# Performance work log

Measured on AMD Instinct MI355X. Metric: run time of the kernel, lower is better.

The kernel has to match this reference:

```python
import jax, jax.numpy as jnp
import numpy as np
from jax import lax

C = 256          # fpn_feats_dim
NC = 20          # num_classes
GROUPS = 16      # GroupNorm groups
EPS = 1e-5       # GroupNorm eps (torch default)
BATCH = 8
LEVELS = [(100, 128), (50, 64), (25, 32)]  # FPN level H,W for 800x1024 image, strides 8/16/32
PRIOR_BIAS = -float(np.log((1 - 0.01) / 0.01))  # ~-4.5951, FCOS prior init


def _conv3(x, w, b):
    # 3x3 stride-1 pad-1 conv, NCHW / OIHW
    y = lax.conv_general_dilated(x, w, (1, 1), 'SAME',
                                 dimension_numbers=('NCHW', 'OIHW', 'NCHW'))
    return y + b[None, :, None, None]


def _gn(x, g, b):
    n, c, h, w = x.shape
    xr = x.reshape(n, GROUPS, c // GROUPS, h, w)
    m = xr.mean(axis=(2, 3, 4), keepdims=True)
    v = xr.var(axis=(2, 3, 4), keepdims=True)
    xr = (xr - m) * lax.rsqrt(v + EPS)
    x = xr.reshape(n, c, h, w)
    return x * g[None, :, None, None] + b[None, :, None, None]


def _forward(feat0, feat1, feat2,
             cls_conv_w, cls_conv_b, cls_gn_g, cls_gn_b, cls_out_w, cls_out_b,
             reg_conv_w, reg_conv_b, reg_gn_g, reg_gn_b,
             reg_out_w, reg_out_b, ctr_w, ctr_b):
    feats = [feat0, feat1, feat2]
    all_cls, all_reg, all_ctr = [], [], []
    for f in feats:
        n = f.shape[0]
        x = f
        for i in range(2):
            x = jax.nn.relu(_gn(_conv3(x, cls_conv_w[i], cls_conv_b[i]),
                                cls_gn_g[i], cls_gn_b[i]))
        logits = _conv3(x, cls_out_w, cls_out_b)           # [N, NC, H, W]
        # view(N,-1,NC,H,W).permute(0,3,4,1,2).reshape(N,-1,NC) == NHWC flatten
        all_cls.append(logits.transpose(0, 2, 3, 1).reshape(n, -1, NC))
        t = f
        for i in range(2):
            t = jax.nn.relu(_gn(_conv3(t, reg_conv_w[i], reg_conv_b[i]),
                                reg_gn_g[i], reg_gn_b[i]))
        # bbox_reg = Sequential(conv, ReLU), then an extra relu in forward (idempotent)
        bbox = jax.nn.relu(jax.nn.relu(_conv3(t, reg_out_w, reg_out_b)))  # [N,4,H,W]
        all_reg.append(bbox.transpose(0, 2, 3, 1).reshape(n, -1, 1))      # [N,H*W*4,1]
        ctr = _conv3(t, ctr_w, ctr_b)                                     # [N,1,H,W]
        all_ctr.append(ctr.transpose(0, 2, 3, 1).reshape(n, -1, 1))       # [N,H*W,1]
    cls_cat = jnp.concatenate(all_cls, axis=1)
    reg_cat = jnp.concatenate(all_reg, axis=1)
    ctr_cat = jnp.concatenate(all_ctr, axis=1)
    return cls_cat, reg_cat, ctr_cat


def setup_inputs() -> dict:
    key = jax.random.key(0)
    ks = jax.random.split(key, 20)
    std = 0.01
    d = {}
    for i, (h, w) in enumerate(LEVELS):
        d[f"feat{i}"] = jax.random.normal(ks[i], (BATCH, C, h, w), jnp.float32)
    # classification head params
    d["cls_conv_w"] = jax.random.normal(ks[3], (2, C, C, 3, 3), jnp.float32) * std
    d["cls_conv_b"] = jnp.zeros((2, C), jnp.float32)
    d["cls_gn_g"] = jnp.ones((2, C), jnp.float32)
    d["cls_gn_b"] = jnp.zeros((2, C), jnp.float32)
    d["cls_out_w"] = jax.random.normal(ks[4], (NC, C, 3, 3), jnp.float32) * std
    d["cls_out_b"] = jnp.full((NC,), PRIOR_BIAS, jnp.float32)
    d["reg_conv_w"] = jax.random.normal(ks[5], (2, C, C, 3, 3), jnp.float32) * std
    d["reg_conv_b"] = jnp.zeros((2, C), jnp.float32)
    d["reg_gn_g"] = jnp.ones((2, C), jnp.float32)
    d["reg_gn_b"] = jnp.zeros((2, C), jnp.float32)
    d["reg_out_w"] = jax.random.normal(ks[6], (4, C, 3, 3), jnp.float32) * std
    d["reg_out_b"] = jnp.zeros((4,), jnp.float32)
    d["ctr_w"] = jax.random.normal(ks[7], (1, C, 3, 3), jnp.float32) * std
    d["ctr_b"] = jnp.zeros((1,), jnp.float32)
    return d


def reference(feat0, feat1, feat2,
              cls_conv_w, cls_conv_b, cls_gn_g, cls_gn_b, cls_out_w, cls_out_b,
              reg_conv_w, reg_conv_b, reg_gn_g, reg_gn_b,
              reg_out_w, reg_out_b, ctr_w, ctr_b):
    return _forward(feat0, feat1, feat2,
                    cls_conv_w, cls_conv_b, cls_gn_g, cls_gn_b, cls_out_w, cls_out_b,
                    reg_conv_w, reg_conv_b, reg_gn_g, reg_gn_b,
                    reg_out_w, reg_out_b, ctr_w, ctr_b)
```

## Files before the change

kernel.cpp:

```cpp
#include <hip/hip_runtime.h>

typedef unsigned short u16;
typedef __attribute__((ext_vector_type(8))) unsigned short ushort8v;
typedef __attribute__((ext_vector_type(8))) short short8v;
typedef __attribute__((ext_vector_type(4))) float floatx4;

__device__ __forceinline__ float bf2f(u16 u) {
    unsigned v = ((unsigned)u) << 16;
    float f;
    __builtin_memcpy(&f, &v, 4);
    return f;
}
__device__ __forceinline__ u16 f2bf(float f) {
    unsigned v;
    __builtin_memcpy(&v, &f, 4);
    unsigned r = (v + 0x7fffu + ((v >> 16) & 1u)) >> 16;
    return (u16)r;
}
__device__ __forceinline__ float ld(const void* p, long i, int isf) {
    return isf ? ((const float*)p)[i] : bf2f(((const u16*)p)[i]);
}
__device__ __forceinline__ void gll16(const void* g, void* l) {
    __builtin_amdgcn_global_load_lds(
        (const __attribute__((address_space(1))) unsigned int*)g,
        (__attribute__((address_space(3))) unsigned int*)l, 16, 0, 0);
}

__global__ void detect_dtype(const u16* __restrict__ gng, int* __restrict__ flag) {
    if (threadIdx.x == 0) flag[0] = (gng[0] == 0x3F80u) ? 0 : 1;
}

__global__ void conv_params(const void* ccb, const void* cgg, const void* cgb,
                            const void* rcb, const void* rgg, const void* rgb,
                            const void* cob, const void* rob, const void* ctb,
                            const int* __restrict__ flag, u16* __restrict__ dst) {
    const int isf = flag[0];
    for (int i = threadIdx.x; i < 3104; i += 256) {
        const void* src; int off;
        if (i < 512)       { src = ccb; off = i; }
        else if (i < 1024) { src = cgg; off = i - 512; }
        else if (i < 1536) { src = cgb; off = i - 1024; }
        else if (i < 2048) { src = rcb; off = i - 1536; }
        else if (i < 2560) { src = rgg; off = i - 2048; }
        else if (i < 3072) { src = rgb; off = i - 2560; }
        else if (i < 3092) { src = cob; off = i - 3072; }
        else if (i < 3096) { src = rob; off = i - 3092; }
        else if (i < 3097) { src = ctb; off = 0; }
        else               { dst[i] = 0; continue; }
        dst[i] = f2bf(ld(src, off, isf));
    }
}

__global__ void prep_w(const void* __restrict__ src, long srcOff,
                       const int* __restrict__ flag, u16* __restrict__ dst,
                       int CoutSrc, int BNr) {
    const int isf = flag[0];
    unsigned e = blockIdx.x * 256 + threadIdx.x;
    unsigned c = e & 31u;
    unsigned r = (e >> 5) % (unsigned)BNr;
    unsigned kc = (e / (32u * BNr)) % 72u;
    unsigned nt = e / (32u * BNr * 72u);
    unsigned co = nt * BNr + r;
    unsigned tap = kc >> 3, ci = (kc & 7u) * 32u + c;
    u16 v = 0;
    if (co < (unsigned)CoutSrc)
        v = f2bf(ld(src, srcOff + (long)(co * 256u + ci) * 9 + tap, isf));
    dst[e] = v;
}

__global__ void prep_w_regctr(const void* __restrict__ wreg, const void* __restrict__ wctr,
                              const int* __restrict__ flag, u16* __restrict__ dst) {
    const int isf = flag[0];
    unsigned e = blockIdx.x * 256 + threadIdx.x;
    unsigned c = e & 31u;
    unsigned r = (e >> 5) & 31u;
    unsigned kc = e / 1024u;
    unsigned tap = kc >> 3, ci = (kc & 7u) * 32u + c;
    u16 v = 0;
    if (r < 4u)       v = f2bf(ld(wreg, (long)(r * 256u + ci) * 9 + tap, isf));
    else if (r == 4u) v = f2bf(ld(wctr, (long)ci * 9 + tap, isf));
    dst[e] = v;
}

__global__ void zero_border(u16* __restrict__ buf, int H, int Wp, int Hp, int NB) {
    const int nb = 2 * Wp + 2 * H;
    unsigned idx = blockIdx.x * 256 + threadIdx.x;
    unsigned ch = idx & 31u;
    unsigned rem = idx >> 5;
    unsigned n = rem / (unsigned)nb;
    unsigned b = rem - n * nb;
    if (n >= (unsigned)NB) return;
    int ppos;
    if ((int)b < Wp) ppos = (int)b;
    else if ((int)b < 2 * Wp) ppos = (Hp - 1) * Wp + ((int)b - Wp);
    else {
        int r = (int)b - 2 * Wp;
        ppos = (1 + (r >> 1)) * Wp + ((r & 1) ? (Wp - 1) : 0);
    }
    ushort8v z = {};
    *(ushort8v*)(buf + ((long)n * (Hp * Wp) + ppos) * 256 + ch * 8) = z;
}

__global__ void nchw_to_nhwc_pad(const void* __restrict__ src, long srcOff,
                                 const int* __restrict__ flag, u16* __restrict__ dst,
                                 int S, int W, int Wp, int HpWp) {
    const int isf = flag[0];
    __shared__ u16 t[64][34];
    const int tid = threadIdx.x;
    const int n = blockIdx.z, ct = blockIdx.y;
    const int s0 = blockIdx.x * 32;
    const long base = srcOff + ((long)(n * 256 + ct * 64)) * S + s0;
#pragma unroll
    for (int i = 0; i < 8; ++i) {
        int c = i * 8 + (tid >> 5);
        t[c][tid & 31] = f2bf(ld(src, base + (long)c * S + (tid & 31), isf));
    }
    __syncthreads();
#pragma unroll
    for (int i = 0; i < 8; ++i) {
        int px = i * 4 + (tid >> 6);
        int s = s0 + px;
        int y = s / W, x = s - y * W;
        dst[((long)n * HpWp + (long)(y + 1) * Wp + (x + 1)) * 256 + ct * 64 + (tid & 63)] =
            t[tid & 63][px];
    }
}

__global__ void gn_stats(const u16* __restrict__ x, float* __restrict__ stats, int S) {
    const int n = blockIdx.x >> 4, g = blockIdx.x & 15;
    const int tid = threadIdx.x;
    float sum = 0.f, sq = 0.f;
    const u16* base = x + (long)n * S * 256 + g * 16 + (tid & 7) * 2;
    for (int p = tid >> 3; p < S; p += 32) {
        unsigned v = *(const unsigned*)(base + (long)p * 256);
        float x0 = bf2f((u16)(v & 0xffffu));
        float x1 = bf2f((u16)(v >> 16));
        sum += x0 + x1;
        sq += x0 * x0 + x1 * x1;
    }
#pragma unroll
    for (int off = 32; off > 0; off >>= 1) {
        sum += __shfl_down(sum, off, 64);
        sq  += __shfl_down(sq, off, 64);
    }
    __shared__ float red[8];
    const int wave = tid >> 6, lane = tid & 63;
    if (lane == 0) { red[wave * 2] = sum; red[wave * 2 + 1] = sq; }
    __syncthreads();
    if (tid == 0) {
        stats[(n * 16 + g) * 2]     = red[0] + red[2] + red[4] + red[6];
        stats[(n * 16 + g) * 2 + 1] = red[1] + red[3] + red[5] + red[7];
    }
}

__global__ void gn_norm_relu(const u16* __restrict__ x, const float* __restrict__ stats,
                             const u16* __restrict__ gam, const u16* __restrict__ bet,
                             u16* __restrict__ outp, int S, int W, int Wp, int HpWp,
                             float invC) {
    unsigned idx = blockIdx.x * 256 + threadIdx.x;
    unsigned c8 = idx & 31u;
    unsigned rem = idx >> 5;
    unsigned p = rem % (unsigned)S;
    unsigned n = rem / (unsigned)S;
    unsigned c0 = c8 * 8u;
    unsigned g = c0 >> 4;
    float sum = stats[(n * 16 + g) * 2], sq = stats[(n * 16 + g) * 2 + 1];
    float mean = sum * invC;
    float var = fmaxf(sq * invC - mean * mean, 0.f);
    float rstd = rsqrtf(var + 1e-5f);
    ushort8v v = *(const ushort8v*)(x + ((long)(n * S + p)) * 256 + c0);
    unsigned y = p / (unsigned)W, xc = p - y * W;
    u16* dst = outp + ((long)n * HpWp + (long)(y + 1) * Wp + (xc + 1)) * 256 + c0;
    ushort8v o;
#pragma unroll
    for (int j = 0; j < 8; ++j) {
        float xv = bf2f(v[j]);
        float r = (xv - mean) * rstd * bf2f(gam[c0 + j]) + bf2f(bet[c0 + j]);
        o[j] = f2bf(fmaxf(r, 0.f));
    }
    *(ushort8v*)dst = o;
}

template <int BN, int MODE>
__global__ __launch_bounds__(256)
void conv_gemm(const u16* __restrict__ Ap, const u16* __restrict__ Wb,
               const u16* __restrict__ bias, const u16* __restrict__ bias2,
               void* __restrict__ outp, long ob1, long ob2,
               const int* __restrict__ dflag,
               int M, int n0, int S, int W, int Wp, int HpWp, int prefS) {
    static_assert(BN == 128 || BN == 32, "");
    constexpr int MI = (BN == 128) ? 4 : 2;
    constexpr int NI = (BN == 128) ? 4 : 2;
    __shared__ __align__(16) u16 ldsA[128 * 32];
    __shared__ __align__(16) u16 ldsB[BN * 32];
    const int tid = threadIdx.x;
    const int lane = tid & 63, wave = tid >> 6;
    const int m0 = blockIdx.x * 128;
    const int nt = blockIdx.y;
    int isf = 0;
    if (MODE != 0) isf = dflag[0];

    const int r0 = 32 * wave + (lane >> 2);
    int mA0 = m0 + r0;        if (mA0 > M - 1) mA0 = M - 1;
    int mA1 = m0 + r0 + 16;   if (mA1 > M - 1) mA1 = M - 1;
    const char* aL0;
    const char* aL1;
    {
        int n8 = mA0 / S, s = mA0 - n8 * S, y = s / W, x = s - y * W;
        aL0 = (const char*)(Ap + ((long)n8 * HpWp + (long)(y + 1) * Wp + (x + 1)) * 256)
              + (lane & 3) * 16;
        n8 = mA1 / S; s = mA1 - n8 * S; y = s / W; x = s - y * W;
        aL1 = (const char*)(Ap + ((long)n8 * HpWp + (long)(y + 1) * Wp + (x + 1)) * 256)
              + (lane & 3) * 16;
    }
    u16* lA0 = ldsA + (32 * wave) * 32;
    u16* lA1 = ldsA + (32 * wave + 16) * 32;

    const u16* b_tile = Wb + (long)nt * 72 * BN * 32;
    const char* bsrc;
    u16* lB0; u16* lB1;
    if (BN == 128) {
        bsrc = (const char*)b_tile + (32 * wave) * 64 + lane * 16;
        lB0 = ldsB + (32 * wave) * 32;
        lB1 = ldsB + (32 * wave + 16) * 32;
    } else {
        bsrc = (const char*)b_tile + wave * 1024 + lane * 16;
        lB0 = ldsB + wave * 16 * 32;
        lB1 = nullptr;
    }

    floatx4 acc[MI][NI] = {};

    const int wm = (BN == 128) ? (wave & 1) * 64 : wave * 32;
    const int wn = (BN == 128) ? (wave >> 1) * 64 : 0;
    const int fr = lane & 15, q = lane >> 4;
    const u16* fA = ldsA + (wm + fr) * 32 + q * 8;
    const u16* fB = ldsB + (wn + fr) * 32 + q * 8;

    for (int kc = 0; kc < 72; ++kc) {
        const int tap = kc >> 3;
        const int ty = tap / 3;
        const int tx = tap - ty * 3;
        const long aoffB = ((long)((ty - 1) * Wp + (tx - 1)) * 256 + (kc & 7) * 32) * 2;
        __syncthreads();
        gll16(aL0 + aoffB, lA0);
        gll16(aL1 + aoffB, lA1);
        if (BN == 128) {
            gll16(bsrc, lB0);
            gll16(bsrc + 1024, lB1);
            bsrc += 8192;
        } else {
            if (wave < 2) gll16(bsrc, lB0);
            bsrc += 2048;
        }
        __syncthreads();
        short8v af[MI], bf[NI];
#pragma unroll
        for (int i = 0; i < MI; ++i) af[i] = *(const short8v*)(fA + i * 16 * 32);
#pragma unroll
        for (int j = 0; j < NI; ++j) bf[j] = *(const short8v*)(fB + j * 16 * 32);
#pragma unroll
        for (int i = 0; i < MI; ++i)
#pragma unroll
            for (int j = 0; j < NI; ++j)
                acc[i][j] = __builtin_amdgcn_mfma_f32_16x16x32_bf16(af[i], bf[j],
                                                                    acc[i][j], 0, 0, 0);
    }

    if (MODE == 0) {
        u16* out = (u16*)outp;
#pragma unroll
        for (int j = 0; j < NI; ++j) {
            const int co = nt * BN + wn + j * 16 + fr;
            const float bv = bf2f(bias[co]);
#pragma unroll
            for (int i = 0; i < MI; ++i) {
#pragma unroll
                for (int r = 0; r < 4; ++r) {
                    const int mg = m0 + wm + i * 16 + q * 4 + r;
                    if (mg < M)
                        out[(long)mg * 256 + co] = f2bf(acc[i][j][r] + bv);
                }
            }
        }
    } else {
#pragma unroll
        for (int i = 0; i < MI; ++i) {
#pragma unroll
            for (int r = 0; r < 4; ++r) {
                const int mg = m0 + wm + i * 16 + q * 4 + r;
                if (mg >= M) continue;
                const int n8 = mg / S;
                const int s = mg - n8 * S;
                const long gi = n0 + n8;
#pragma unroll
                for (int j = 0; j < NI; ++j) {
                    const int co = wn + j * 16 + fr;
                    const float v = acc[i][j][r];
                    long oi = -1;
                    float val = 0.f;
                    if (MODE == 1) {
                        if (co < 20) {
                            oi = ob1 + gi * 336000 + (long)(prefS + s) * 20 + co;
                            val = v + bf2f(bias[co]);
                        }
                    } else {
                        if (co < 4) {
                            oi = ob1 + gi * 67200 + (long)(prefS + s) * 4 + co;
                            val = fmaxf(v + bf2f(bias[co]), 0.f);
                        } else if (co == 4) {
                            oi = ob2 + gi * 16800 + (prefS + s);
                            val = v + bf2f(bias2[0]);
                        }
                    }
                    if (oi >= 0) {
                        if (isf) ((float*)outp)[oi] = val;
                        else     ((u16*)outp)[oi] = f2bf(val);
                    }
                }
            }
        }
    }
}

extern "C" void kernel_launch(void* const* d_in, const int* in_sizes, int n_in,
                              void* d_out, int out_size, void* d_ws, size_t ws_size,
                              hipStream_t stream) {
    (void)in_sizes; (void)n_in; (void)out_size;
    const void* feat[3]   = {d_in[0], d_in[1], d_in[2]};
    const void* cls_conv_w = d_in[3];
    const void* cls_conv_b = d_in[4];
    const void* cls_gn_g   = d_in[5];
    const void* cls_gn_b   = d_in[6];
    const void* cls_out_w  = d_in[7];
    const void* cls_out_b  = d_in[8];
    const void* reg_conv_w = d_in[9];
    const void* reg_conv_b = d_in[10];
    const void* reg_gn_g   = d_in[11];
    const void* reg_gn_b   = d_in[12];
    const void* reg_out_w  = d_in[13];
    const void* reg_out_b  = d_in[14];
    const void* ctr_w      = d_in[15];
    const void* ctr_b      = d_in[16];

    char* ws = (char*)d_ws;
    int*  flag     = (int*)ws;
    u16*  params   = (u16*)(ws + 1024);
    u16*  Wb       = (u16*)(ws + 8192);
    float* stats   = (float*)(ws + 5021696);
    const size_t base = 5022720;
    const size_t per_img = 6789120ull + 6553600ull + 6789120ull;
    int NB = 8;
    while (NB > 1 && base + (size_t)NB * per_img > ws_size) NB >>= 1;
    u16* feat_pad  = (u16*)(ws + base);
    u16* conv_out  = (u16*)(ws + base + (size_t)NB * 6789120ull);
    u16* norm_pad  = (u16*)(ws + base + (size_t)NB * (6789120ull + 6553600ull));

    detect_dtype<<<1, 64, 0, stream>>>((const u16*)cls_gn_g, flag);
    conv_params<<<1, 256, 0, stream>>>(cls_conv_b, cls_gn_g, cls_gn_b,
                                       reg_conv_b, reg_gn_g, reg_gn_b,
                                       cls_out_b, reg_out_b, ctr_b, flag, params);
    prep_w<<<2304, 256, 0, stream>>>(cls_conv_w, 0,      flag, Wb + 0,       256, 128);
    prep_w<<<2304, 256, 0, stream>>>(cls_conv_w, 589824, flag, Wb + 589824,  256, 128);
    prep_w<<<2304, 256, 0, stream>>>(reg_conv_w, 0,      flag, Wb + 1179648, 256, 128);
    prep_w<<<2304, 256, 0, stream>>>(reg_conv_w, 589824, flag, Wb + 1769472, 256, 128);
    prep_w<<<288,  256, 0, stream>>>(cls_out_w,  0,      flag, Wb + 2359296, 20, 32);
    prep_w_regctr<<<288, 256, 0, stream>>>(reg_out_w, ctr_w, flag, Wb + 2433024);

    const int Hs[3] = {100, 50, 25}, Wss[3] = {128, 64, 32};
    const int prefSs[3] = {0, 12800, 16000};

    for (int l = 0; l < 3; ++l) {
        const int H = Hs[l], W = Wss[l], S = H * W;
        const int Hp = H + 2, Wp = W + 2, HpWp = Hp * Wp;
        const int prefS = prefSs[l];
        const int nb = 2 * Wp + 2 * H;
        const float invC = 1.0f / (16.0f * (float)S);

        for (int n0 = 0; n0 < 8; n0 += NB) {
            const int M = NB * S;
            const int mtiles = (M + 127) / 128;
            const int zb_blocks = (NB * nb * 32 + 255) / 256;

            zero_border<<<zb_blocks, 256, 0, stream>>>(feat_pad, H, Wp, Hp, NB);
            zero_border<<<zb_blocks, 256, 0, stream>>>(norm_pad, H, Wp, Hp, NB);
            nchw_to_nhwc_pad<<<dim3(S / 32, 4, NB), 256, 0, stream>>>(
                feat[l], (long)n0 * 256 * S, flag, feat_pad, S, W, Wp, HpWp);

            conv_gemm<128, 0><<<dim3(mtiles, 2), 256, 0, stream>>>(
                feat_pad, Wb + 0, params + 0, nullptr, conv_out, 0, 0, flag,
                M, n0, S, W, Wp, HpWp, 0);
            gn_stats<<<NB * 16, 256, 0, stream>>>(conv_out, stats, S);
            gn_norm_relu<<<M / 8, 256, 0, stream>>>(conv_out, stats, params + 512,
                                                    params + 1024, norm_pad,
                                                    S, W, Wp, HpWp, invC);
            conv_gemm<128, 0><<<dim3(mtiles, 2), 256, 0, stream>>>(
                norm_pad, Wb + 589824, params + 256, nullptr, conv_out, 0, 0, flag,
                M, n0, S, W, Wp, HpWp, 0);
            gn_stats<<<NB * 16, 256, 0, stream>>>(conv_out, stats, S);
            gn_norm_relu<<<M / 8, 256, 0, stream>>>(conv_out, stats, params + 512 + 256,
                                                    params + 1024 + 256, norm_pad,
                                                    S, W, Wp, HpWp, invC);
            conv_gemm<32, 1><<<dim3(mtiles, 1), 256, 0, stream>>>(
                norm_pad, Wb + 2359296, params + 3072, nullptr, d_out, 0, 0, flag,
                M, n0, S, W, Wp, HpWp, prefS);

            conv_gemm<128, 0><<<dim3(mtiles, 2), 256, 0, stream>>>(
                feat_pad, Wb + 1179648, params + 1536, nullptr, conv_out, 0, 0, flag,
                M, n0, S, W, Wp, HpWp, 0);
            gn_stats<<<NB * 16, 256, 0, stream>>>(conv_out, stats, S);
            gn_norm_relu<<<M / 8, 256, 0, stream>>>(conv_out, stats, params + 2048,
                                                    params + 2560, norm_pad,
                                                    S, W, Wp, HpWp, invC);
            conv_gemm<128, 0><<<dim3(mtiles, 2), 256, 0, stream>>>(
                norm_pad, Wb + 1769472, params + 1536 + 256, nullptr, conv_out, 0, 0, flag,
                M, n0, S, W, Wp, HpWp, 0);
            gn_stats<<<NB * 16, 256, 0, stream>>>(conv_out, stats, S);
            gn_norm_relu<<<M / 8, 256, 0, stream>>>(conv_out, stats, params + 2048 + 256,
                                                    params + 2560 + 256, norm_pad,
                                                    S, W, Wp, HpWp, invC);
            conv_gemm<32, 2><<<dim3(mtiles, 1), 256, 0, stream>>>(
                norm_pad, Wb + 2433024, params + 3092, params + 3096,
                d_out, 2688000, 3225600, flag,
                M, n0, S, W, Wp, HpWp, prefS);
        }
    }
}
```

Baseline: 2.528 ms.

## Load conv GEMM fragments directly from global memory and remap workgroups across XCDs

The conv implicit-GEMM kernel no longer stages A and B tiles through LDS with global_load_lds and barriers. Each lane now loads its MFMA fragments straight from global memory, relying on caches for reuse across waves. Workgroup IDs are also remapped so that consecutive tiles land on the same XCD, which improves L2 locality. The trade-off is more redundant global/L2 traffic, since each wave reloads shared tiles, in exchange for removing LDS round-trips and synchronisation.

After: 3.536 ms. 1.4x slower.

```diff
diff --git a/kernel.cpp b/kernel.cpp
--- a/kernel.cpp
+++ b/kernel.cpp
@@ -19,11 +19,6 @@
 }
 __device__ __forceinline__ float ld(const void* p, long i, int isf) {
     return isf ? ((const float*)p)[i] : bf2f(((const u16*)p)[i]);
-}
-__device__ __forceinline__ void gll16(const void* g, void* l) {
-    __builtin_amdgcn_global_load_lds(
-        (const __attribute__((address_space(1))) unsigned int*)g,
-        (__attribute__((address_space(3))) unsigned int*)l, 16, 0, 0);
 }
 
 __global__ void detect_dtype(const u16* __restrict__ gng, int* __restrict__ flag) {
@@ -191,80 +186,65 @@
     static_assert(BN == 128 || BN == 32, "");
     constexpr int MI = (BN == 128) ? 4 : 2;
     constexpr int NI = (BN == 128) ? 4 : 2;
-    __shared__ __align__(16) u16 ldsA[128 * 32];
-    __shared__ __align__(16) u16 ldsB[BN * 32];
     const int tid = threadIdx.x;
     const int lane = tid & 63, wave = tid >> 6;
-    const int m0 = blockIdx.x * 128;
-    const int nt = blockIdx.y;
+
+    const unsigned NTg = gridDim.y;
+    const unsigned nwg = gridDim.x * NTg;
+    const unsigned lin = blockIdx.y * gridDim.x + blockIdx.x;
+    const unsigned qq = nwg >> 3, rr = nwg & 7u;
+    const unsigned xcd = lin & 7u, pos = lin >> 3;
+    const unsigned wg =
+        (xcd < rr ? xcd * (qq + 1u) : rr * (qq + 1u) + (xcd - rr) * qq) + pos;
+    const int nt = (int)(wg % NTg);
+    const int m0 = (int)(wg / NTg) * 128;
+
     int isf = 0;
     if (MODE != 0) isf = dflag[0];
-
-    const int r0 = 32 * wave + (lane >> 2);
-    int mA0 = m0 + r0;        if (mA0 > M - 1) mA0 = M - 1;
-    int mA1 = m0 + r0 + 16;   if (mA1 > M - 1) mA1 = M - 1;
-    const char* aL0;
-    const char* aL1;
-    {
-        int n8 = mA0 / S, s = mA0 - n8 * S, y = s / W, x = s - y * W;
-        aL0 = (const char*)(Ap + ((long)n8 * HpWp + (long)(y + 1) * Wp + (x + 1)) * 256)
-              + (lane & 3) * 16;
-        n8 = mA1 / S; s = mA1 - n8 * S; y = s / W; x = s - y * W;
-        aL1 = (const char*)(Ap + ((long)n8 * HpWp + (long)(y + 1) * Wp + (x + 1)) * 256)
-              + (lane & 3) * 16;
-    }
-    u16* lA0 = ldsA + (32 * wave) * 32;
-    u16* lA1 = ldsA + (32 * wave + 16) * 32;
-
-    const u16* b_tile = Wb + (long)nt * 72 * BN * 32;
-    const char* bsrc;
-    u16* lB0; u16* lB1;
-    if (BN == 128) {
-        bsrc = (const char*)b_tile + (32 * wave) * 64 + lane * 16;
-        lB0 = ldsB + (32 * wave) * 32;
-        lB1 = ldsB + (32 * wave + 16) * 32;
-    } else {
-        bsrc = (const char*)b_tile + wave * 1024 + lane * 16;
-        lB0 = ldsB + wave * 16 * 32;
-        lB1 = nullptr;
-    }
-
-    floatx4 acc[MI][NI] = {};
 
     const int wm = (BN == 128) ? (wave & 1) * 64 : wave * 32;
     const int wn = (BN == 128) ? (wave >> 1) * 64 : 0;
     const int fr = lane & 15, q = lane >> 4;
-    const u16* fA = ldsA + (wm + fr) * 32 + q * 8;
-    const u16* fB = ldsB + (wn + fr) * 32 + q * 8;
-
-    for (int kc = 0; kc < 72; ++kc) {
-        const int tap = kc >> 3;
-        const int ty = tap / 3;
-        const int tx = tap - ty * 3;
-        const long aoffB = ((long)((ty - 1) * Wp + (tx - 1)) * 256 + (kc & 7) * 32) * 2;
-        __syncthreads();
-        gll16(aL0 + aoffB, lA0);
-        gll16(aL1 + aoffB, lA1);
-        if (BN == 128) {
-            gll16(bsrc, lB0);
-            gll16(bsrc + 1024, lB1);
-            bsrc += 8192;
-        } else {
-            if (wave < 2) gll16(bsrc, lB0);
-            bsrc += 2048;
+
+    const char* A8 = (const char*)Ap;
+    int abase[MI];
+#pragma unroll
+    for (int i = 0; i < MI; ++i) {
+        int mg = m0 + wm + i * 16 + fr;
+        if (mg > M - 1) mg = M - 1;
+        int n8 = mg / S, s = mg - n8 * S, y = s / W, x = s - y * W;
+        abase[i] = ((n8 * HpWp + (y + 1) * Wp) + (x + 1)) * 512 + q * 16;
+    }
+    const char* B8 = (const char*)(Wb + (long)nt * 72 * BN * 32);
+    int bbase[NI];
+#pragma unroll
+    for (int j = 0; j < NI; ++j)
+        bbase[j] = (wn + j * 16 + fr) * 64 + q * 16;
+
+    floatx4 acc[MI][NI] = {};
+
+#pragma unroll 1
+    for (int tap = 0; tap < 9; ++tap) {
+        const int ty = tap / 3, tx = tap - ty * 3;
+        const int aoff = ((ty - 1) * Wp + (tx - 1)) * 512;
+        const int boff = tap * 8 * BN * 64;
+#pragma unroll
+        for (int ci = 0; ci < 8; ++ci) {
+            short8v af[MI], bf[NI];
+#pragma unroll
+            for (int i = 0; i < MI; ++i)
+                af[i] = *(const short8v*)(A8 + (long)(abase[i] + aoff) + ci * 64);
+#pragma unroll
+            for (int j = 0; j < NI; ++j)
+                bf[j] = *(const short8v*)(B8 + (long)(bbase[j] + boff)
+                                          + (long)ci * (BN * 64));
+#pragma unroll
+            for (int i = 0; i < MI; ++i)
+#pragma unroll
+                for (int j = 0; j < NI; ++j)
+                    acc[i][j] = __builtin_amdgcn_mfma_f32_16x16x32_bf16(
+                        af[i], bf[j], acc[i][j], 0, 0, 0);
         }
-        __syncthreads();
-        short8v af[MI], bf[NI];
-#pragma unroll
-        for (int i = 0; i < MI; ++i) af[i] = *(const short8v*)(fA + i * 16 * 32);
-#pragma unroll
-        for (int j = 0; j < NI; ++j) bf[j] = *(const short8v*)(fB + j * 16 * 32);
-#pragma unroll
-        for (int i = 0; i < MI; ++i)
-#pragma unroll
-            for (int j = 0; j < NI; ++j)
-                acc[i][j] = __builtin_amdgcn_mfma_f32_16x16x32_bf16(af[i], bf[j],
-                                                                    acc[i][j], 0, 0, 0);
     }
 
     if (MODE == 0) {
```

## Double-buffer LDS tiles in conv GEMM and remap blocks across XCDs

Applied to the files above, without the earlier changes.

The implicit-GEMM conv kernel now keeps two LDS buffers for A and B. It issues the global-to-LDS loads for the next K chunk before the MFMA work on the current chunk, and uses one waitcnt plus barrier per iteration instead of two syncthreads. It also remaps the linear workgroup id so consecutive tiles land on the same XCD, with the N tile varying fastest, to improve L2 reuse of the weights and input rows. In exchange LDS use doubles, which may lower occupancy, and the new barrier placement has to be correct so a buffer is not overwritten while another wave is still reading it.

Result: no change. 2.523 ms (-0.2%).

```diff
diff --git a/kernel.cpp b/kernel.cpp
--- a/kernel.cpp
+++ b/kernel.cpp
@@ -191,12 +191,23 @@
     static_assert(BN == 128 || BN == 32, "");
     constexpr int MI = (BN == 128) ? 4 : 2;
     constexpr int NI = (BN == 128) ? 4 : 2;
-    __shared__ __align__(16) u16 ldsA[128 * 32];
-    __shared__ __align__(16) u16 ldsB[BN * 32];
+    constexpr int ASZ = 128 * 32;
+    constexpr int BSZ = BN * 32;
+    __shared__ __align__(16) u16 ldsA[2 * ASZ];
+    __shared__ __align__(16) u16 ldsB[2 * BSZ];
     const int tid = threadIdx.x;
     const int lane = tid & 63, wave = tid >> 6;
-    const int m0 = blockIdx.x * 128;
-    const int nt = blockIdx.y;
+
+    const unsigned NTg = gridDim.y;
+    const unsigned nwg = gridDim.x * NTg;
+    const unsigned lin = blockIdx.y * gridDim.x + blockIdx.x;
+    const unsigned qq = nwg >> 3, rr = nwg & 7u;
+    const unsigned xcd = lin & 7u, pos = lin >> 3;
+    const unsigned wg =
+        (xcd < rr ? xcd * (qq + 1u) : rr * (qq + 1u) + (xcd - rr) * qq) + pos;
+    const int nt = (int)(wg % NTg);
+    const int m0 = (int)(wg / NTg) * 128;
+
     int isf = 0;
     if (MODE != 0) isf = dflag[0];
 
@@ -217,17 +228,33 @@
     u16* lA1 = ldsA + (32 * wave + 16) * 32;
 
     const u16* b_tile = Wb + (long)nt * 72 * BN * 32;
-    const char* bsrc;
+    const char* bsrc0;
     u16* lB0; u16* lB1;
     if (BN == 128) {
-        bsrc = (const char*)b_tile + (32 * wave) * 64 + lane * 16;
+        bsrc0 = (const char*)b_tile + (32 * wave) * 64 + lane * 16;
         lB0 = ldsB + (32 * wave) * 32;
         lB1 = ldsB + (32 * wave + 16) * 32;
     } else {
-        bsrc = (const char*)b_tile + wave * 1024 + lane * 16;
+        bsrc0 = (const char*)b_tile + wave * 1024 + lane * 16;
         lB0 = ldsB + wave * 16 * 32;
         lB1 = nullptr;
     }
+
+    auto STAGE = [&](int kc, int p) {
+        const int tap = kc >> 3;
+        const int ty = tap / 3;
+        const int tx = tap - ty * 3;
+        const long aoffB = ((long)((ty - 1) * Wp + (tx - 1)) * 256 + (kc & 7) * 32) * 2;
+        gll16(aL0 + aoffB, lA0 + p * ASZ);
+        gll16(aL1 + aoffB, lA1 + p * ASZ);
+        if (BN == 128) {
+            const char* bs = bsrc0 + (long)kc * 8192;
+            gll16(bs, lB0 + p * BSZ);
+            gll16(bs + 1024, lB1 + p * BSZ);
+        } else {
+            if (wave < 2) gll16(bsrc0 + (long)kc * 2048, lB0 + p * BSZ);
+        }
+    };
 
     floatx4 acc[MI][NI] = {};
 
@@ -237,28 +264,38 @@
     const u16* fA = ldsA + (wm + fr) * 32 + q * 8;
     const u16* fB = ldsB + (wn + fr) * 32 + q * 8;
 
-    for (int kc = 0; kc < 72; ++kc) {
-        const int tap = kc >> 3;
-        const int ty = tap / 3;
-        const int tx = tap - ty * 3;
-        const long aoffB = ((long)((ty - 1) * Wp + (tx - 1)) * 256 + (kc & 7) * 32) * 2;
-        __syncthreads();
-        gll16(aL0 + aoffB, lA0);
-        gll16(aL1 + aoffB, lA1);
-        if (BN == 128) {
-            gll16(bsrc, lB0);
-            gll16(bsrc + 1024, lB1);
-            bsrc += 8192;
-        } else {
-            if (wave < 2) gll16(bsrc, lB0);
-            bsrc += 2048;
-        }
-        __syncthreads();
+    STAGE(0, 0);
+    asm volatile("s_waitcnt vmcnt(0)" ::: "memory");
+    __builtin_amdgcn_s_barrier();
+
+#pragma unroll 1
+    for (int kc = 0; kc < 71; ++kc) {
+        const int p = kc & 1;
+        STAGE(kc + 1, p ^ 1);
         short8v af[MI], bf[NI];
-#pragma unroll
-        for (int i = 0; i < MI; ++i) af[i] = *(const short8v*)(fA + i * 16 * 32);
-#pragma unroll
-        for (int j = 0; j < NI; ++j) bf[j] = *(const short8v*)(fB + j * 16 * 32);
+        const u16* fAp = fA + p * ASZ;
+        const u16* fBp = fB + p * BSZ;
+#pragma unroll
+        for (int i = 0; i < MI; ++i) af[i] = *(const short8v*)(fAp + i * 16 * 32);
+#pragma unroll
+        for (int j = 0; j < NI; ++j) bf[j] = *(const short8v*)(fBp + j * 16 * 32);
+#pragma unroll
+        for (int i = 0; i < MI; ++i)
+#pragma unroll
+            for (int j = 0; j < NI; ++j)
+                acc[i][j] = __builtin_amdgcn_mfma_f32_16x16x32_bf16(af[i], bf[j],
+                                                                    acc[i][j], 0, 0, 0);
+        asm volatile("s_waitcnt vmcnt(0)" ::: "memory");
+        __builtin_amdgcn_s_barrier();
+    }
+    {
+        short8v af[MI], bf[NI];
+        const u16* fAp = fA + ASZ;
+        const u16* fBp = fB + BSZ;
+#pragma unroll
+        for (int i = 0; i < MI; ++i) af[i] = *(const short8v*)(fAp + i * 16 * 32);
+#pragma unroll
+        for (int j = 0; j < NI; ++j) bf[j] = *(const short8v*)(fBp + j * 16 * 32);
 #pragma unroll
         for (int i = 0; i < MI; ++i)
 #pragma unroll
```
